# Performance work log

Measured on AMD Instinct MI355X. Metric: run time of the kernel, lower is better.

## Reference

```python
import jax, jax.numpy as jnp
import numpy as np

N, T, F, H = 20000, 64, 32, 64
E = 640000
G1, G2 = 64, 32


def _lstm_layer(x_seq, Wih, Whh, bih, bhh):
    # x_seq: [N, T, Fin] -> hs [N, T, H], PyTorch gate order i,f,g,o
    n, _, _ = x_seq.shape
    h_dim = Whh.shape[1]
    h0 = jnp.zeros((n, h_dim), x_seq.dtype)
    c0 = jnp.zeros((n, h_dim), x_seq.dtype)

    def step(carry, xt):
        h, c = carry
        gates = xt @ Wih.T + h @ Whh.T + bih + bhh
        i, f, g, o = jnp.split(gates, 4, axis=-1)
        c = jax.nn.sigmoid(f) * c + jax.nn.sigmoid(i) * jnp.tanh(g)
        h = jax.nn.sigmoid(o) * jnp.tanh(c)
        return (h, c), h

    (_, _), hs = jax.lax.scan(step, (h0, c0), jnp.swapaxes(x_seq, 0, 1))
    return jnp.swapaxes(hs, 0, 1)


def _gcn(h, src, dst, W, b):
    # GCNConv (PyG default): add self-loops, symmetric deg^-1/2 normalization
    n = h.shape[0]
    loop = jnp.arange(n)
    s = jnp.concatenate([src, loop])
    d = jnp.concatenate([dst, loop])
    deg = jax.ops.segment_sum(jnp.ones_like(d, dtype=h.dtype), d, num_segments=n)
    dinv = jnp.where(deg > 0, deg ** -0.5, 0.0)
    norm = dinv[s] * dinv[d]
    xw = h @ W                      # [n, out]
    msg = xw[s] * norm[:, None]     # gather on source nodes
    return jax.ops.segment_sum(msg, d, num_segments=n) + b


def setup_inputs() -> dict:
    key = jax.random.key(0)
    ks = jax.random.split(key, 16)
    s = 0.1
    inp = {
        "x": jax.random.normal(ks[0], (N, T, F), jnp.float32),
        "stock_ids": jax.random.randint(ks[1], (N,), 0, N),
        "edge_index": jax.random.randint(ks[2], (2, E), 0, N),
        # LSTM layer 0
        "Wih0": jax.random.normal(ks[3], (4 * H, F), jnp.float32) * s,
        "Whh0": jax.random.normal(ks[4], (4 * H, H), jnp.float32) * s,
        "bih0": jnp.zeros((4 * H,), jnp.float32),
        "bhh0": jnp.zeros((4 * H,), jnp.float32),
        # LSTM layer 1
        "Wih1": jax.random.normal(ks[5], (4 * H, H), jnp.float32) * s,
        "Whh1": jax.random.normal(ks[6], (4 * H, H), jnp.float32) * s,
        "bih1": jnp.zeros((4 * H,), jnp.float32),
        "bhh1": jnp.zeros((4 * H,), jnp.float32),
        # GCN layers
        "gcn1_W": jax.random.normal(ks[7], (H, G1), jnp.float32) * s,
        "gcn1_b": jnp.zeros((G1,), jnp.float32),
        "gcn2_W": jax.random.normal(ks[8], (G1, G2), jnp.float32) * s,
        "gcn2_b": jnp.zeros((G2,), jnp.float32),
        # head
        "fc_W": jax.random.normal(ks[9], (1, G2), jnp.float32) * s,
        "fc_b": jnp.zeros((1,), jnp.float32),
    }
    return inp


def reference(x, stock_ids, edge_index, Wih0, Whh0, bih0, bhh0,
              Wih1, Whh1, bih1, bhh1, gcn1_W, gcn1_b, gcn2_W, gcn2_b,
              fc_W, fc_b):
    # 2-layer LSTM (eval mode: inter-layer dropout is identity)
    h1 = _lstm_layer(x, Wih0, Whh0, bih0, bhh0)
    h2 = _lstm_layer(h1, Wih1, Whh1, bih1, bhh1)
    h = h2[:, -1, :]                              # [N, H]
    src, dst = edge_index[0], edge_index[1]
    g = jax.nn.relu(_gcn(h, src, dst, gcn1_W, gcn1_b))
    g = jax.nn.relu(_gcn(g, src, dst, gcn2_W, gcn2_b))
    node_features = g[stock_ids]                  # [B, 32]
    out = node_features @ fc_W.T + fc_b           # [B, 1]
    return out.squeeze(-1)
```

## Files before the change

### kernel.cpp

```cpp
#include <hip/hip_runtime.h>
#include <math.h>

#define TT 64
#define FF 32
#define HH 64
#define NN 16
#define GG1 64
#define GG2 32

typedef float f32x4 __attribute__((ext_vector_type(4)));
typedef short bf16x8 __attribute__((ext_vector_type(8)));

__device__ __forceinline__ float fexp2(float x){ return __builtin_amdgcn_exp2f(x); }
__device__ __forceinline__ float frcp (float x){ return __builtin_amdgcn_rcpf(x); }
__device__ __forceinline__ float sigm (float v){ return frcp(1.0f + fexp2(-1.442695041f*v)); }
__device__ __forceinline__ float ftanh(float v){ return fmaf(-2.0f, frcp(1.0f + fexp2(2.885390082f*v)), 1.0f); }

__device__ __forceinline__ float xor8(float v){
  int a = __builtin_bit_cast(int, v);
  int b = __builtin_amdgcn_update_dpp(0, a, 0x128, 0xF, 0xF, true);
  return __builtin_bit_cast(float, b);
}

__device__ __forceinline__ unsigned short bf16rn(float x){
  unsigned u = __builtin_bit_cast(unsigned, x);
  return (unsigned short)((u + 0x7FFFu + ((u >> 16) & 1u)) >> 16);
}
__device__ __forceinline__ void split2(float x, unsigned short& h, unsigned short& l){
  unsigned u = __builtin_bit_cast(unsigned, x);
  unsigned hr = (u + 0x7FFFu + ((u >> 16) & 1u)) & 0xFFFF0000u;
  h = (unsigned short)(hr >> 16);
  l = bf16rn(x - __builtin_bit_cast(float, hr));
}

#define PIN(v) asm volatile("" : "+v"(v))
#define MFMA(acc, a, b) (acc) = __builtin_amdgcn_mfma_f32_16x16x32_bf16((a), (b), (acc), 0, 0, 0)

__device__ __forceinline__ void wsplit(const float* p, bf16x8& hi, bf16x8& lo){
  float4 a = *(const float4*)p;
  float4 b = *(const float4*)(p + 4);
  unsigned short h, s;
  split2(a.x,h,s); hi[0]=(short)h; lo[0]=(short)s;
  split2(a.y,h,s); hi[1]=(short)h; lo[1]=(short)s;
  split2(a.z,h,s); hi[2]=(short)h; lo[2]=(short)s;
  split2(a.w,h,s); hi[3]=(short)h; lo[3]=(short)s;
  split2(b.x,h,s); hi[4]=(short)h; lo[4]=(short)s;
  split2(b.y,h,s); hi[5]=(short)h; lo[5]=(short)s;
  split2(b.z,h,s); hi[6]=(short)h; lo[6]=(short)s;
  split2(b.w,h,s); hi[7]=(short)h; lo[7]=(short)s;
}

__global__ __launch_bounds__(512, 2)
void lstm_mfma(const float* __restrict__ x,
    const float* __restrict__ Wih0, const float* __restrict__ Whh0,
    const float* __restrict__ bih0, const float* __restrict__ bhh0,
    const float* __restrict__ Wih1, const float* __restrict__ Whh1,
    const float* __restrict__ bih1, const float* __restrict__ bhh1,
    float* __restrict__ hout, int n)
{
  const int tid = threadIdx.x;
  const int w   = tid >> 6;
  const int l   = tid & 63;
  const int lr  = l & 15;
  const int lg  = l >> 4;
  const int nA  = blockIdx.x * NN;
  int avail = n - nA; if (avail > NN) avail = NN;

  __shared__ short Ax[2][2][16][40];
  __shared__ short H0[2][2][16][88];
  __shared__ short H1[2][2][16][88];

  const int jm   = lr & 7;
  const int col0 = (lr < 8) ? (8*w + jm) : (64  + 8*w + jm);
  const int col1 = (lr < 8) ? (128 + 8*w + jm) : (192 + 8*w + jm);

  bf16x8 W0h[2][3], W0l[2][3], W1h[2][4], W1l[2][4];
  float bias0[2], bias1[2];
#pragma unroll
  for (int h = 0; h < 2; ++h){
    const int col = h ? col1 : col0;
    wsplit(Wih0 + col*FF + 8*lg,      W0h[h][0], W0l[h][0]);
    wsplit(Whh0 + col*HH + 8*lg,      W0h[h][1], W0l[h][1]);
    wsplit(Whh0 + col*HH + 32 + 8*lg, W0h[h][2], W0l[h][2]);
    wsplit(Wih1 + col*HH + 8*lg,      W1h[h][0], W1l[h][0]);
    wsplit(Wih1 + col*HH + 32 + 8*lg, W1h[h][1], W1l[h][1]);
    wsplit(Whh1 + col*HH + 8*lg,      W1h[h][2], W1l[h][2]);
    wsplit(Whh1 + col*HH + 32 + 8*lg, W1h[h][3], W1l[h][3]);
    bias0[h] = bih0[col] + bhh0[col];
    bias1[h] = bih1[col] + bhh1[col];
  }
#pragma unroll
  for (int h = 0; h < 2; ++h){
#pragma unroll
    for (int k = 0; k < 3; ++k){ PIN(W0h[h][k]); PIN(W0l[h][k]); }
#pragma unroll
    for (int k = 0; k < 4; ++k){ PIN(W1h[h][k]); PIN(W1l[h][k]); }
  }

  {
    short* p0 = &H0[0][0][0][0];
    short* p1 = &H1[0][0][0][0];
    for (int i = tid; i < 2*2*16*88; i += 512){ p0[i] = 0; p1[i] = 0; }
    const int xnd = tid >> 5, xf = tid & 31;
    float v = (xnd < avail) ? x[((size_t)(nA+xnd)*TT + 0)*FF + xf] : 0.0f;
    unsigned short hh, hl; split2(v, hh, hl);
    Ax[0][0][xnd][xf] = (short)hh;
    Ax[0][1][xnd][xf] = (short)hl;
  }
  const int na = 4*lg + ((lr < 8) ? 0 : 2);
  const int nb = na + 1;
  const int m  = 8*w + jm;
  const bool lo8 = (lr < 8);
  float c0a = 0.0f, c0b = 0.0f, c1a = 0.0f, c1b = 0.0f;
  __syncthreads();

  for (int t = 0; t < TT; ++t){
    const int rd0 = (t & 1) ^ 1;
    const int wr0 =  t & 1;
    const int rd1 =  t & 1;
    const int wr1 = (t & 1) ^ 1;

    const int xnd = tid >> 5, xf = tid & 31;
    const int tp = t + 1;
    float xv = 0.0f;
    if (tp < TT && xnd < avail) xv = x[((size_t)(nA+xnd)*TT + tp)*FF + xf];

    bf16x8 axh  = *(const bf16x8*)&Ax[t&1][0][lr][8*lg];
    bf16x8 axl  = *(const bf16x8*)&Ax[t&1][1][lr][8*lg];
    bf16x8 h0ah = *(const bf16x8*)&H0[rd0][0][lr][8*lg];
    bf16x8 h0al = *(const bf16x8*)&H0[rd0][1][lr][8*lg];
    bf16x8 h0bh = *(const bf16x8*)&H0[rd0][0][lr][32+8*lg];
    bf16x8 h0bl = *(const bf16x8*)&H0[rd0][1][lr][32+8*lg];

    f32x4 acc0 = {bias0[0], bias0[0], bias0[0], bias0[0]};
    f32x4 acc1 = {bias0[1], bias0[1], bias0[1], bias0[1]};
    MFMA(acc0, axl,  W0h[0][0]); MFMA(acc0, axh,  W0l[0][0]); MFMA(acc0, axh,  W0h[0][0]);
    MFMA(acc1, axl,  W0h[1][0]); MFMA(acc1, axh,  W0l[1][0]); MFMA(acc1, axh,  W0h[1][0]);
    MFMA(acc0, h0al, W0h[0][1]); MFMA(acc0, h0ah, W0l[0][1]); MFMA(acc0, h0ah, W0h[0][1]);
    MFMA(acc1, h0al, W0h[1][1]); MFMA(acc1, h0ah, W0l[1][1]); MFMA(acc1, h0ah, W0h[1][1]);
    MFMA(acc0, h0bl, W0h[0][2]); MFMA(acc0, h0bh, W0l[0][2]); MFMA(acc0, h0bh, W0h[0][2]);
    MFMA(acc1, h0bl, W0h[1][2]); MFMA(acc1, h0bh, W0l[1][2]); MFMA(acc1, h0bh, W0h[1][2]);

    f32x4 acd0, acd1;
    if (t > 0){
      bf16x8 h1ah = *(const bf16x8*)&H1[rd1][0][lr][8*lg];
      bf16x8 h1al = *(const bf16x8*)&H1[rd1][1][lr][8*lg];
      bf16x8 h1bh = *(const bf16x8*)&H1[rd1][0][lr][32+8*lg];
      bf16x8 h1bl = *(const bf16x8*)&H1[rd1][1][lr][32+8*lg];
      acd0 = (f32x4){bias1[0], bias1[0], bias1[0], bias1[0]};
      acd1 = (f32x4){bias1[1], bias1[1], bias1[1], bias1[1]};
      MFMA(acd0, h0al, W1h[0][0]); MFMA(acd0, h0ah, W1l[0][0]); MFMA(acd0, h0ah, W1h[0][0]);
      MFMA(acd1, h0al, W1h[1][0]); MFMA(acd1, h0ah, W1l[1][0]); MFMA(acd1, h0ah, W1h[1][0]);
      MFMA(acd0, h0bl, W1h[0][1]); MFMA(acd0, h0bh, W1l[0][1]); MFMA(acd0, h0bh, W1h[0][1]);
      MFMA(acd1, h0bl, W1h[1][1]); MFMA(acd1, h0bh, W1l[1][1]); MFMA(acd1, h0bh, W1h[1][1]);
      MFMA(acd0, h1al, W1h[0][2]); MFMA(acd0, h1ah, W1l[0][2]); MFMA(acd0, h1ah, W1h[0][2]);
      MFMA(acd1, h1al, W1h[1][2]); MFMA(acd1, h1ah, W1l[1][2]); MFMA(acd1, h1ah, W1h[1][2]);
      MFMA(acd0, h1bl, W1h[0][3]); MFMA(acd0, h1bh, W1l[0][3]); MFMA(acd0, h1bh, W1h[0][3]);
      MFMA(acd1, h1bl, W1h[1][3]); MFMA(acd1, h1bh, W1l[1][3]); MFMA(acd1, h1bh, W1h[1][3]);
    }

    if (tp < TT){
      unsigned short hh, hl; split2(xv, hh, hl);
      Ax[tp&1][0][xnd][xf] = (short)hh;
      Ax[tp&1][1][xnd][xf] = (short)hl;
    }

    {
      f32x4 s0, s1;
      s0[0]=xor8(acc0[0]); s0[1]=xor8(acc0[1]); s0[2]=xor8(acc0[2]); s0[3]=xor8(acc0[3]);
      s1[0]=xor8(acc1[0]); s1[1]=xor8(acc1[1]); s1[2]=xor8(acc1[2]); s1[3]=xor8(acc1[3]);
      float gi_a = lo8 ? acc0[0] : s0[2],  gi_b = lo8 ? acc0[1] : s0[3];
      float gf_a = lo8 ? s0[0] : acc0[2],  gf_b = lo8 ? s0[1] : acc0[3];
      float gg_a = lo8 ? acc1[0] : s1[2],  gg_b = lo8 ? acc1[1] : s1[3];
      float go_a = lo8 ? s1[0] : acc1[2],  go_b = lo8 ? s1[1] : acc1[3];
      c0a = sigm(gf_a)*c0a + sigm(gi_a)*ftanh(gg_a);
      float ha = sigm(go_a)*ftanh(c0a);
      c0b = sigm(gf_b)*c0b + sigm(gi_b)*ftanh(gg_b);
      float hb = sigm(go_b)*ftanh(c0b);
      unsigned short hh, hl;
      split2(ha, hh, hl); H0[wr0][0][na][m] = (short)hh; H0[wr0][1][na][m] = (short)hl;
      split2(hb, hh, hl); H0[wr0][0][nb][m] = (short)hh; H0[wr0][1][nb][m] = (short)hl;
    }
    if (t > 0){
      f32x4 s0, s1;
      s0[0]=xor8(acd0[0]); s0[1]=xor8(acd0[1]); s0[2]=xor8(acd0[2]); s0[3]=xor8(acd0[3]);
      s1[0]=xor8(acd1[0]); s1[1]=xor8(acd1[1]); s1[2]=xor8(acd1[2]); s1[3]=xor8(acd1[3]);
      float gi_a = lo8 ? acd0[0] : s0[2],  gi_b = lo8 ? acd0[1] : s0[3];
      float gf_a = lo8 ? s0[0] : acd0[2],  gf_b = lo8 ? s0[1] : acd0[3];
      float gg_a = lo8 ? acd1[0] : s1[2],  gg_b = lo8 ? acd1[1] : s1[3];
      float go_a = lo8 ? s1[0] : acd1[2],  go_b = lo8 ? s1[1] : acd1[3];
      c1a = sigm(gf_a)*c1a + sigm(gi_a)*ftanh(gg_a);
      float ha = sigm(go_a)*ftanh(c1a);
      c1b = sigm(gf_b)*c1b + sigm(gi_b)*ftanh(gg_b);
      float hb = sigm(go_b)*ftanh(c1b);
      unsigned short hh, hl;
      split2(ha, hh, hl); H1[wr1][0][na][m] = (short)hh; H1[wr1][1][na][m] = (short)hl;
      split2(hb, hh, hl); H1[wr1][0][nb][m] = (short)hh; H1[wr1][1][nb][m] = (short)hl;
    }
    __syncthreads();
  }

  {
    const int rd0 = (TT-1) & 1;
    const int rd1 =  TT & 1;
    bf16x8 h0ah = *(const bf16x8*)&H0[rd0][0][lr][8*lg];
    bf16x8 h0al = *(const bf16x8*)&H0[rd0][1][lr][8*lg];
    bf16x8 h0bh = *(const bf16x8*)&H0[rd0][0][lr][32+8*lg];
    bf16x8 h0bl = *(const bf16x8*)&H0[rd0][1][lr][32+8*lg];
    bf16x8 h1ah = *(const bf16x8*)&H1[rd1][0][lr][8*lg];
    bf16x8 h1al = *(const bf16x8*)&H1[rd1][1][lr][8*lg];
    bf16x8 h1bh = *(const bf16x8*)&H1[rd1][0][lr][32+8*lg];
    bf16x8 h1bl = *(const bf16x8*)&H1[rd1][1][lr][32+8*lg];
    f32x4 acd0 = {bias1[0], bias1[0], bias1[0], bias1[0]};
    f32x4 acd1 = {bias1[1], bias1[1], bias1[1], bias1[1]};
    MFMA(acd0, h0al, W1h[0][0]); MFMA(acd0, h0ah, W1l[0][0]); MFMA(acd0, h0ah, W1h[0][0]);
    MFMA(acd1, h0al, W1h[1][0]); MFMA(acd1, h0ah, W1l[1][0]); MFMA(acd1, h0ah, W1h[1][0]);
    MFMA(acd0, h0bl, W1h[0][1]); MFMA(acd0, h0bh, W1l[0][1]); MFMA(acd0, h0bh, W1h[0][1]);
    MFMA(acd1, h0bl, W1h[1][1]); MFMA(acd1, h0bh, W1l[1][1]); MFMA(acd1, h0bh, W1h[1][1]);
    MFMA(acd0, h1al, W1h[0][2]); MFMA(acd0, h1ah, W1l[0][2]); MFMA(acd0, h1ah, W1h[0][2]);
    MFMA(acd1, h1al, W1h[1][2]); MFMA(acd1, h1ah, W1l[1][2]); MFMA(acd1, h1ah, W1h[1][2]);
    MFMA(acd0, h1bl, W1h[0][3]); MFMA(acd0, h1bh, W1l[0][3]); MFMA(acd0, h1bh, W1h[0][3]);
    MFMA(acd1, h1bl, W1h[1][3]); MFMA(acd1, h1bh, W1l[1][3]); MFMA(acd1, h1bh, W1h[1][3]);

    f32x4 s0, s1;
    s0[0]=xor8(acd0[0]); s0[1]=xor8(acd0[1]); s0[2]=xor8(acd0[2]); s0[3]=xor8(acd0[3]);
    s1[0]=xor8(acd1[0]); s1[1]=xor8(acd1[1]); s1[2]=xor8(acd1[2]); s1[3]=xor8(acd1[3]);
    float gi_a = lo8 ? acd0[0] : s0[2],  gi_b = lo8 ? acd0[1] : s0[3];
    float gf_a = lo8 ? s0[0] : acd0[2],  gf_b = lo8 ? s0[1] : acd0[3];
    float gg_a = lo8 ? acd1[0] : s1[2],  gg_b = lo8 ? acd1[1] : s1[3];
    float go_a = lo8 ? s1[0] : acd1[2],  go_b = lo8 ? s1[1] : acd1[3];
    c1a = sigm(gf_a)*c1a + sigm(gi_a)*ftanh(gg_a);
    float ha = sigm(go_a)*ftanh(c1a);
    c1b = sigm(gf_b)*c1b + sigm(gi_b)*ftanh(gg_b);
    float hb = sigm(go_b)*ftanh(c1b);
    if (nA + na < n) hout[(size_t)(nA+na)*HH + m] = ha;
    if (nA + nb < n) hout[(size_t)(nA+nb)*HH + m] = hb;
  }
}

__global__ void k_count(const int* __restrict__ dst, int E, int* __restrict__ cnt)
{
  int e = blockIdx.x * blockDim.x + threadIdx.x;
  if (e < E) atomicAdd(&cnt[dst[e]], 1);
}

__global__ void k_scan_build(const int* __restrict__ cnt, int n,
                             int* __restrict__ offs, int* __restrict__ cursor,
                             float* __restrict__ dinv)
{
  __shared__ int part[1024];
  const int tid = threadIdx.x;
  const int per = (n + 1023) >> 10;
  const int base = tid * per;
  int s = 0;
  for (int i = 0; i < per; ++i) { int idx = base + i; if (idx < n) s += cnt[idx]; }
  part[tid] = s;
  __syncthreads();
  for (int off = 1; off < 1024; off <<= 1) {
    int v = 0;
    if (tid >= off) v = part[tid - off];
    __syncthreads();
    part[tid] += v;
    __syncthreads();
  }
  int run = part[tid] - s;
  for (int i = 0; i < per; ++i) {
    int idx = base + i;
    if (idx < n) {
      offs[idx] = run; cursor[idx] = run;
      int c = cnt[idx];
      dinv[idx] = 1.0f / sqrtf((float)(c + 1));
      run += c;
    }
  }
}

__global__ void k_fill(const int* __restrict__ src, const int* __restrict__ dst,
                       int E, int* __restrict__ cursor, int* __restrict__ csr)
{
  int e = blockIdx.x * blockDim.x + threadIdx.x;
  if (e < E) {
    int d = dst[e];
    int pos = atomicAdd(&cursor[d], 1);
    csr[pos] = src[e];
  }
}

template <int K, int M>
__global__ void k_xw(const float* __restrict__ A, const float* __restrict__ W,
                     float* __restrict__ out, int n)
{
  int idx = blockIdx.x * blockDim.x + threadIdx.x;
  int row = idx / M, col = idx % M;
  if (row >= n) return;
  const float* a = A + (size_t)row * K;
  float acc = 0.0f;
#pragma unroll
  for (int k = 0; k < K; ++k) acc = fmaf(a[k], W[k*M + col], acc);
  out[(size_t)row*M + col] = acc;
}

template <int FD>
__global__ void k_agg(const float* __restrict__ xw, const int* __restrict__ offs,
                      const int* __restrict__ cnt, const int* __restrict__ csr,
                      const float* __restrict__ dinv, const float* __restrict__ b,
                      float* __restrict__ out, int n)
{
  int gidx = blockIdx.x * blockDim.x + threadIdx.x;
  int node = gidx / FD, lane = gidx % FD;
  if (node >= n) return;
  const float di = dinv[node];
  float acc = xw[(size_t)node*FD + lane] * di * di;
  const int s0 = offs[node], e0 = s0 + cnt[node];
  for (int p = s0; p < e0; ++p) {
    int s = csr[p];
    acc = fmaf(xw[(size_t)s*FD + lane], dinv[s] * di, acc);
  }
  out[(size_t)node*FD + lane] = fmaxf(acc + b[lane], 0.0f);
}

__global__ void k_fc(const float* __restrict__ g2, const int* __restrict__ sid,
                     const float* __restrict__ fcW, const float* __restrict__ fcb,
                     float* __restrict__ out, int n)
{
  int i = blockIdx.x * blockDim.x + threadIdx.x;
  if (i >= n) return;
  const float* row = g2 + (size_t)sid[i] * GG2;
  float acc = fcb[0];
#pragma unroll
  for (int f = 0; f < GG2; ++f) acc = fmaf(row[f], fcW[f], acc);
  out[i] = acc;
}

extern "C" void kernel_launch(void* const* d_in, const int* in_sizes, int n_in,
                              void* d_out, int out_size, void* d_ws, size_t ws_size,
                              hipStream_t stream)
{
  const float* x    = (const float*)d_in[0];
  const int*   sid  = (const int*)  d_in[1];
  const int*   eidx = (const int*)  d_in[2];
  const float* Wih0 = (const float*)d_in[3];
  const float* Whh0 = (const float*)d_in[4];
  const float* bih0 = (const float*)d_in[5];
  const float* bhh0 = (const float*)d_in[6];
  const float* Wih1 = (const float*)d_in[7];
  const float* Whh1 = (const float*)d_in[8];
  const float* bih1 = (const float*)d_in[9];
  const float* bhh1 = (const float*)d_in[10];
  const float* g1W  = (const float*)d_in[11];
  const float* g1b  = (const float*)d_in[12];
  const float* g2W  = (const float*)d_in[13];
  const float* g2b  = (const float*)d_in[14];
  const float* fcW  = (const float*)d_in[15];
  const float* fcb  = (const float*)d_in[16];

  const int n = in_sizes[1];
  const int E = in_sizes[2] / 2;
  float* out = (float*)d_out;

  char* w = (char*)d_ws;
  auto carve = [&](size_t bytes) -> void* {
    void* p = (void*)w; w += (bytes + 255) & ~(size_t)255; return p;
  };
  float* hfin   = (float*)carve((size_t)n * HH * 4);
  int*   cnt    = (int*)  carve((size_t)n * 4);
  int*   offs   = (int*)  carve((size_t)n * 4);
  int*   cursor = (int*)  carve((size_t)n * 4);
  float* dinv   = (float*)carve((size_t)n * 4);
  int*   csr    = (int*)  carve((size_t)E * 4);
  float* xw1    = (float*)carve((size_t)n * GG1 * 4);
  float* g1     = (float*)carve((size_t)n * GG1 * 4);
  float* xw2    = (float*)carve((size_t)n * GG2 * 4);
  float* g2     = (float*)carve((size_t)n * GG2 * 4);

  const int* src = eidx;
  const int* dst = eidx + E;

  lstm_mfma<<<(n + NN - 1) / NN, 512, 0, stream>>>(x, Wih0, Whh0, bih0, bhh0,
                                                   Wih1, Whh1, bih1, bhh1, hfin, n);

  hipMemsetAsync(cnt, 0, (size_t)n * 4, stream);
  k_count<<<(E + 255) / 256, 256, 0, stream>>>(dst, E, cnt);
  k_scan_build<<<1, 1024, 0, stream>>>(cnt, n, offs, cursor, dinv);
  k_fill<<<(E + 255) / 256, 256, 0, stream>>>(src, dst, E, cursor, csr);

  k_xw<HH, GG1><<<((size_t)n * GG1 + 255) / 256, 256, 0, stream>>>(hfin, g1W, xw1, n);
  k_agg<GG1><<<((size_t)n * GG1 + 255) / 256, 256, 0, stream>>>(xw1, offs, cnt, csr, dinv, g1b, g1, n);

  k_xw<GG1, GG2><<<((size_t)n * GG2 + 255) / 256, 256, 0, stream>>>(g1, g2W, xw2, n);
  k_agg<GG2><<<((size_t)n * GG2 + 255) / 256, 256, 0, stream>>>(xw2, offs, cnt, csr, dinv, g2b, g2, n);

  k_fc<<<(n + 255) / 256, 256, 0, stream>>>(g2, sid, fcW, fcb, out, n);
}
```

Baseline: 692.9 us.

## Fold gate biases into activations, pack bf16 splits, prioritize MFMA, fuse GCN agg with xw2

```diff
diff --git a/kernel.cpp b/kernel.cpp
--- a/kernel.cpp
+++ b/kernel.cpp
@@ -13,8 +13,16 @@
 
 __device__ __forceinline__ float fexp2(float x){ return __builtin_amdgcn_exp2f(x); }
 __device__ __forceinline__ float frcp (float x){ return __builtin_amdgcn_rcpf(x); }
-__device__ __forceinline__ float sigm (float v){ return frcp(1.0f + fexp2(-1.442695041f*v)); }
-__device__ __forceinline__ float ftanh(float v){ return fmaf(-2.0f, frcp(1.0f + fexp2(2.885390082f*v)), 1.0f); }
+#define L2E 1.442695041f
+__device__ __forceinline__ float sigm_nb(float v, float nb){
+  return frcp(1.0f + fexp2(fmaf(v, -L2E, nb)));
+}
+__device__ __forceinline__ float tanh_b(float v, float b2){
+  return fmaf(-2.0f, frcp(1.0f + fexp2(fmaf(v, 2.0f*L2E, b2))), 1.0f);
+}
+__device__ __forceinline__ float tanh0(float v){
+  return fmaf(-2.0f, frcp(1.0f + fexp2(2.0f*L2E*v)), 1.0f);
+}
 
 __device__ __forceinline__ float xor8(float v){
   int a = __builtin_bit_cast(int, v);
@@ -31,6 +39,13 @@
   unsigned hr = (u + 0x7FFFu + ((u >> 16) & 1u)) & 0xFFFF0000u;
   h = (unsigned short)(hr >> 16);
   l = bf16rn(x - __builtin_bit_cast(float, hr));
+}
+__device__ __forceinline__ void split_pk(float a, float b, unsigned& hi2, unsigned& lo2){
+  asm("v_cvt_pk_bf16_f32 %0, %1, %2" : "=v"(hi2) : "v"(a), "v"(b));
+  float ha = __builtin_bit_cast(float, hi2 << 16);
+  float hb = __builtin_bit_cast(float, hi2 & 0xFFFF0000u);
+  float la = a - ha, lb = b - hb;
+  asm("v_cvt_pk_bf16_f32 %0, %1, %2" : "=v"(lo2) : "v"(la), "v"(lb));
 }
 
 #define PIN(v) asm volatile("" : "+v"(v))
@@ -71,11 +86,11 @@
   __shared__ short H1[2][2][16][88];
 
   const int jm   = lr & 7;
-  const int col0 = (lr < 8) ? (8*w + jm) : (64  + 8*w + jm);
-  const int col1 = (lr < 8) ? (128 + 8*w + jm) : (192 + 8*w + jm);
+  const bool lo8 = (lr < 8);
+  const int col0 = lo8 ? (8*w + jm) : (64  + 8*w + jm);
+  const int col1 = lo8 ? (128 + 8*w + jm) : (192 + 8*w + jm);
 
   bf16x8 W0h[2][3], W0l[2][3], W1h[2][4], W1l[2][4];
-  float bias0[2], bias1[2];
 #pragma unroll
   for (int h = 0; h < 2; ++h){
     const int col = h ? col1 : col0;
@@ -86,8 +101,6 @@
     wsplit(Wih1 + col*HH + 32 + 8*lg, W1h[h][1], W1l[h][1]);
     wsplit(Whh1 + col*HH + 8*lg,      W1h[h][2], W1l[h][2]);
     wsplit(Whh1 + col*HH + 32 + 8*lg, W1h[h][3], W1l[h][3]);
-    bias0[h] = bih0[col] + bhh0[col];
-    bias1[h] = bih1[col] + bhh1[col];
   }
 #pragma unroll
   for (int h = 0; h < 2; ++h){
@@ -96,6 +109,16 @@
 #pragma unroll
     for (int k = 0; k < 4; ++k){ PIN(W1h[h][k]); PIN(W1l[h][k]); }
   }
+
+  const int m  = 8*w + jm;
+  const float nb_i0 = -L2E      * (bih0[m      ] + bhh0[m      ]);
+  const float nb_f0 = -L2E      * (bih0[m +  64] + bhh0[m +  64]);
+  const float b2_g0 =  2.0f*L2E * (bih0[m + 128] + bhh0[m + 128]);
+  const float nb_o0 = -L2E      * (bih0[m + 192] + bhh0[m + 192]);
+  const float nb_i1 = -L2E      * (bih1[m      ] + bhh1[m      ]);
+  const float nb_f1 = -L2E      * (bih1[m +  64] + bhh1[m +  64]);
+  const float b2_g1 =  2.0f*L2E * (bih1[m + 128] + bhh1[m + 128]);
+  const float nb_o1 = -L2E      * (bih1[m + 192] + bhh1[m + 192]);
 
   {
     short* p0 = &H0[0][0][0][0];
@@ -107,11 +130,10 @@
     Ax[0][0][xnd][xf] = (short)hh;
     Ax[0][1][xnd][xf] = (short)hl;
   }
-  const int na = 4*lg + ((lr < 8) ? 0 : 2);
+  const int na = 4*lg + (lo8 ? 0 : 2);
   const int nb = na + 1;
-  const int m  = 8*w + jm;
-  const bool lo8 = (lr < 8);
   float c0a = 0.0f, c0b = 0.0f, c1a = 0.0f, c1b = 0.0f;
+  const f32x4 Z = {0.f, 0.f, 0.f, 0.f};
   __syncthreads();
 
   for (int t = 0; t < TT; ++t){
@@ -132,10 +154,12 @@
     bf16x8 h0bh = *(const bf16x8*)&H0[rd0][0][lr][32+8*lg];
     bf16x8 h0bl = *(const bf16x8*)&H0[rd0][1][lr][32+8*lg];
 
-    f32x4 acc0 = {bias0[0], bias0[0], bias0[0], bias0[0]};
-    f32x4 acc1 = {bias0[1], bias0[1], bias0[1], bias0[1]};
-    MFMA(acc0, axl,  W0h[0][0]); MFMA(acc0, axh,  W0l[0][0]); MFMA(acc0, axh,  W0h[0][0]);
-    MFMA(acc1, axl,  W0h[1][0]); MFMA(acc1, axh,  W0l[1][0]); MFMA(acc1, axh,  W0h[1][0]);
+    __builtin_amdgcn_s_setprio(1);
+    f32x4 acc0, acc1;
+    acc0 = __builtin_amdgcn_mfma_f32_16x16x32_bf16(axl, W0h[0][0], Z, 0, 0, 0);
+    acc1 = __builtin_amdgcn_mfma_f32_16x16x32_bf16(axl, W0h[1][0], Z, 0, 0, 0);
+    MFMA(acc0, axh,  W0l[0][0]); MFMA(acc0, axh,  W0h[0][0]);
+    MFMA(acc1, axh,  W0l[1][0]); MFMA(acc1, axh,  W0h[1][0]);
     MFMA(acc0, h0al, W0h[0][1]); MFMA(acc0, h0ah, W0l[0][1]); MFMA(acc0, h0ah, W0h[0][1]);
     MFMA(acc1, h0al, W0h[1][1]); MFMA(acc1, h0ah, W0l[1][1]); MFMA(acc1, h0ah, W0h[1][1]);
     MFMA(acc0, h0bl, W0h[0][2]); MFMA(acc0, h0bh, W0l[0][2]); MFMA(acc0, h0bh, W0h[0][2]);
@@ -147,10 +171,10 @@
       bf16x8 h1al = *(const bf16x8*)&H1[rd1][1][lr][8*lg];
       bf16x8 h1bh = *(const bf16x8*)&H1[rd1][0][lr][32+8*lg];
       bf16x8 h1bl = *(const bf16x8*)&H1[rd1][1][lr][32+8*lg];
-      acd0 = (f32x4){bias1[0], bias1[0], bias1[0], bias1[0]};
-      acd1 = (f32x4){bias1[1], bias1[1], bias1[1], bias1[1]};
-      MFMA(acd0, h0al, W1h[0][0]); MFMA(acd0, h0ah, W1l[0][0]); MFMA(acd0, h0ah, W1h[0][0]);
-      MFMA(acd1, h0al, W1h[1][0]); MFMA(acd1, h0ah, W1l[1][0]); MFMA(acd1, h0ah, W1h[1][0]);
+      acd0 = __builtin_amdgcn_mfma_f32_16x16x32_bf16(h0al, W1h[0][0], Z, 0, 0, 0);
+      acd1 = __builtin_amdgcn_mfma_f32_16x16x32_bf16(h0al, W1h[1][0], Z, 0, 0, 0);
+      MFMA(acd0, h0ah, W1l[0][0]); MFMA(acd0, h0ah, W1h[0][0]);
+      MFMA(acd1, h0ah, W1l[1][0]); MFMA(acd1, h0ah, W1h[1][0]);
       MFMA(acd0, h0bl, W1h[0][1]); MFMA(acd0, h0bh, W1l[0][1]); MFMA(acd0, h0bh, W1h[0][1]);
       MFMA(acd1, h0bl, W1h[1][1]); MFMA(acd1, h0bh, W1l[1][1]); MFMA(acd1, h0bh, W1h[1][1]);
       MFMA(acd0, h1al, W1h[0][2]); MFMA(acd0, h1ah, W1l[0][2]); MFMA(acd0, h1ah, W1h[0][2]);
@@ -158,6 +182,7 @@
       MFMA(acd0, h1bl, W1h[0][3]); MFMA(acd0, h1bh, W1l[0][3]); MFMA(acd0, h1bh, W1h[0][3]);
       MFMA(acd1, h1bl, W1h[1][3]); MFMA(acd1, h1bh, W1l[1][3]); MFMA(acd1, h1bh, W1h[1][3]);
     }
+    __builtin_amdgcn_s_setprio(0);
 
     if (tp < TT){
       unsigned short hh, hl; split2(xv, hh, hl);
@@ -173,13 +198,15 @@
       float gf_a = lo8 ? s0[0] : acc0[2],  gf_b = lo8 ? s0[1] : acc0[3];
       float gg_a = lo8 ? acc1[0] : s1[2],  gg_b = lo8 ? acc1[1] : s1[3];
       float go_a = lo8 ? s1[0] : acc1[2],  go_b = lo8 ? s1[1] : acc1[3];
-      c0a = sigm(gf_a)*c0a + sigm(gi_a)*ftanh(gg_a);
-      float ha = sigm(go_a)*ftanh(c0a);
-      c0b = sigm(gf_b)*c0b + sigm(gi_b)*ftanh(gg_b);
-      float hb = sigm(go_b)*ftanh(c0b);
-      unsigned short hh, hl;
-      split2(ha, hh, hl); H0[wr0][0][na][m] = (short)hh; H0[wr0][1][na][m] = (short)hl;
-      split2(hb, hh, hl); H0[wr0][0][nb][m] = (short)hh; H0[wr0][1][nb][m] = (short)hl;
+      c0a = sigm_nb(gf_a, nb_f0)*c0a + sigm_nb(gi_a, nb_i0)*tanh_b(gg_a, b2_g0);
+      float ha = sigm_nb(go_a, nb_o0)*tanh0(c0a);
+      c0b = sigm_nb(gf_b, nb_f0)*c0b + sigm_nb(gi_b, nb_i0)*tanh_b(gg_b, b2_g0);
+      float hb = sigm_nb(go_b, nb_o0)*tanh0(c0b);
+      unsigned hi2, lo2; split_pk(ha, hb, hi2, lo2);
+      H0[wr0][0][na][m] = (short)(hi2 & 0xFFFF);
+      H0[wr0][0][nb][m] = (short)(hi2 >> 16);
+      H0[wr0][1][na][m] = (short)(lo2 & 0xFFFF);
+      H0[wr0][1][nb][m] = (short)(lo2 >> 16);
     }
     if (t > 0){
       f32x4 s0, s1;
@@ -189,13 +216,15 @@
       float gf_a = lo8 ? s0[0] : acd0[2],  gf_b = lo8 ? s0[1] : acd0[3];
       float gg_a = lo8 ? acd1[0] : s1[2],  gg_b = lo8 ? acd1[1] : s1[3];
       float go_a = lo8 ? s1[0] : acd1[2],  go_b = lo8 ? s1[1] : acd1[3];
-      c1a = sigm(gf_a)*c1a + sigm(gi_a)*ftanh(gg_a);
-      float ha = sigm(go_a)*ftanh(c1a);
-      c1b = sigm(gf_b)*c1b + sigm(gi_b)*ftanh(gg_b);
-      float hb = sigm(go_b)*ftanh(c1b);
-      unsigned short hh, hl;
-      split2(ha, hh, hl); H1[wr1][0][na][m] = (short)hh; H1[wr1][1][na][m] = (short)hl;
-      split2(hb, hh, hl); H1[wr1][0][nb][m] = (short)hh; H1[wr1][1][nb][m] = (short)hl;
+      c1a = sigm_nb(gf_a, nb_f1)*c1a + sigm_nb(gi_a, nb_i1)*tanh_b(gg_a, b2_g1);
+      float ha = sigm_nb(go_a, nb_o1)*tanh0(c1a);
+      c1b = sigm_nb(gf_b, nb_f1)*c1b + sigm_nb(gi_b, nb_i1)*tanh_b(gg_b, b2_g1);
+      float hb = sigm_nb(go_b, nb_o1)*tanh0(c1b);
+      unsigned hi2, lo2; split_pk(ha, hb, hi2, lo2);
+      H1[wr1][0][na][m] = (short)(hi2 & 0xFFFF);
+      H1[wr1][0][nb][m] = (short)(hi2 >> 16);
+      H1[wr1][1][na][m] = (short)(lo2 & 0xFFFF);
+      H1[wr1][1][nb][m] = (short)(lo2 >> 16);
     }
     __syncthreads();
   }
@@ -211,10 +240,10 @@
     bf16x8 h1al = *(const bf16x8*)&H1[rd1][1][lr][8*lg];
     bf16x8 h1bh = *(const bf16x8*)&H1[rd1][0][lr][32+8*lg];
     bf16x8 h1bl = *(const bf16x8*)&H1[rd1][1][lr][32+8*lg];
-    f32x4 acd0 = {bias1[0], bias1[0], bias1[0], bias1[0]};
-    f32x4 acd1 = {bias1[1], bias1[1], bias1[1], bias1[1]};
-    MFMA(acd0, h0al, W1h[0][0]); MFMA(acd0, h0ah, W1l[0][0]); MFMA(acd0, h0ah, W1h[0][0]);
-    MFMA(acd1, h0al, W1h[1][0]); MFMA(acd1, h0ah, W1l[1][0]); MFMA(acd1, h0ah, W1h[1][0]);
+    f32x4 acd0 = __builtin_amdgcn_mfma_f32_16x16x32_bf16(h0al, W1h[0][0], Z, 0, 0, 0);
+    f32x4 acd1 = __builtin_amdgcn_mfma_f32_16x16x32_bf16(h0al, W1h[1][0], Z, 0, 0, 0);
+    MFMA(acd0, h0ah, W1l[0][0]); MFMA(acd0, h0ah, W1h[0][0]);
+    MFMA(acd1, h0ah, W1l[1][0]); MFMA(acd1, h0ah, W1h[1][0]);
     MFMA(acd0, h0bl, W1h[0][1]); MFMA(acd0, h0bh, W1l[0][1]); MFMA(acd0, h0bh, W1h[0][1]);
     MFMA(acd1, h0bl, W1h[1][1]); MFMA(acd1, h0bh, W1l[1][1]); MFMA(acd1, h0bh, W1h[1][1]);
     MFMA(acd0, h1al, W1h[0][2]); MFMA(acd0, h1ah, W1l[0][2]); MFMA(acd0, h1ah, W1h[0][2]);
@@ -229,10 +258,10 @@
     float gf_a = lo8 ? s0[0] : acd0[2],  gf_b = lo8 ? s0[1] : acd0[3];
     float gg_a = lo8 ? acd1[0] : s1[2],  gg_b = lo8 ? acd1[1] : s1[3];
     float go_a = lo8 ? s1[0] : acd1[2],  go_b = lo8 ? s1[1] : acd1[3];
-    c1a = sigm(gf_a)*c1a + sigm(gi_a)*ftanh(gg_a);
-    float ha = sigm(go_a)*ftanh(c1a);
-    c1b = sigm(gf_b)*c1b + sigm(gi_b)*ftanh(gg_b);
-    float hb = sigm(go_b)*ftanh(c1b);
+    c1a = sigm_nb(gf_a, nb_f1)*c1a + sigm_nb(gi_a, nb_i1)*tanh_b(gg_a, b2_g1);
+    float ha = sigm_nb(go_a, nb_o1)*tanh0(c1a);
+    c1b = sigm_nb(gf_b, nb_f1)*c1b + sigm_nb(gi_b, nb_i1)*tanh_b(gg_b, b2_g1);
+    float hb = sigm_nb(go_b, nb_o1)*tanh0(c1b);
     if (nA + na < n) hout[(size_t)(nA+na)*HH + m] = ha;
     if (nA + nb < n) hout[(size_t)(nA+nb)*HH + m] = hb;
   }
@@ -298,6 +327,37 @@
 #pragma unroll
   for (int k = 0; k < K; ++k) acc = fmaf(a[k], W[k*M + col], acc);
   out[(size_t)row*M + col] = acc;
+}
+
+__global__ void k_agg_x2(const float* __restrict__ xw, const int* __restrict__ offs,
+                         const int* __restrict__ cnt, const int* __restrict__ csr,
+                         const float* __restrict__ dinv, const float* __restrict__ b,
+                         const float* __restrict__ W2,
+                         float* __restrict__ g1out, float* __restrict__ xw2out, int n)
+{
+  __shared__ float sg[4][GG1];
+  const int nd   = threadIdx.x >> 6;
+  const int lane = threadIdx.x & 63;
+  const int node = blockIdx.x * 4 + nd;
+  if (node < n) {
+    const float di = dinv[node];
+    float acc = xw[(size_t)node*GG1 + lane] * di * di;
+    const int s0 = offs[node], e0 = s0 + cnt[node];
+    for (int p = s0; p < e0; ++p) {
+      int s = csr[p];
+      acc = fmaf(xw[(size_t)s*GG1 + lane], dinv[s] * di, acc);
+    }
+    float val = fmaxf(acc + b[lane], 0.0f);
+    g1out[(size_t)node*GG1 + lane] = val;
+    sg[nd][lane] = val;
+  }
+  __syncthreads();
+  if (node < n && lane < GG2) {
+    float a2 = 0.0f;
+#pragma unroll
+    for (int k = 0; k < GG1; ++k) a2 = fmaf(sg[nd][k], W2[k*GG2 + lane], a2);
+    xw2out[(size_t)node*GG2 + lane] = a2;
+  }
 }
 
 template <int FD>
@@ -385,9 +445,8 @@
   k_fill<<<(E + 255) / 256, 256, 0, stream>>>(src, dst, E, cursor, csr);
 
   k_xw<HH, GG1><<<((size_t)n * GG1 + 255) / 256, 256, 0, stream>>>(hfin, g1W, xw1, n);
-  k_agg<GG1><<<((size_t)n * GG1 + 255) / 256, 256, 0, stream>>>(xw1, offs, cnt, csr, dinv, g1b, g1, n);
-
-  k_xw<GG1, GG2><<<((size_t)n * GG2 + 255) / 256, 256, 0, stream>>>(g1, g2W, xw2, n);
+  k_agg_x2<<<(n + 3) / 4, 256, 0, stream>>>(xw1, offs, cnt, csr, dinv, g1b, g2W, g1, xw2, n);
+
   k_agg<GG2><<<((size_t)n * GG2 + 255) / 256, 256, 0, stream>>>(xw2, offs, cnt, csr, dinv, g2b, g2, n);
 
   k_fc<<<(n + 255) / 256, 256, 0, stream>>>(g2, sid, fcW, fcb, out, n);
```

Result: no change. 696.5 us (+0.5%).
